# Kernel optimization log

Hardware: AMD Instinct MI355X
Metric: run time of the kernel (lower is better)

Reference implementation:

```python
import jax, jax.numpy as jnp
import numpy as np

V, EMB, H, N, E, B = 100000, 300, 64, 20000, 160000, 4096
L, T = 2, 3  # layer_timesteps = [3, 3]


def setup_inputs() -> dict:
    key = jax.random.key(0)
    ks = jax.random.split(key, 24)
    ri = lambda k, shape, hi: jax.random.randint(k, shape, 0, hi)
    rn = lambda k, shape, s=0.05: (jax.random.normal(k, shape, dtype=jnp.float32) * s)
    emb_table = rn(ks[7], (V, EMB), 0.1).at[0].set(0.0)  # padding_idx=0 row is zeros
    return {
        'emb_ind0': ri(ks[0], (N,), V),
        'emb_ind1': ri(ks[1], (N,), V),
        'adj0': ri(ks[2], (E, 2), N),
        'adj1': ri(ks[3], (E, 2), N),
        'prop_ind0': ri(ks[4], (B,), N),
        'prop_ind1': ri(ks[5], (B,), N),
        'labels': ri(ks[6], (B,), 2),
        'emb_table': emb_table,
        'proj_W': rn(ks[8], (EMB, H)),   # emb_proj weight (stored input-major)
        'proj_b': jnp.zeros((H,), jnp.float32),
        'msg_W': rn(ks[9], (L, H, H)),   # per-layer edge-type-0 message linear
        'msg_b': jnp.zeros((L, H), jnp.float32),
        'gru_Wih': rn(ks[10], (L, 3 * H, H)),
        'gru_Whh': rn(ks[11], (L, 3 * H, H)),
        'gru_bih': jnp.zeros((L, 3 * H), jnp.float32),
        'gru_bhh': jnp.zeros((L, 3 * H), jnp.float32),
        'cla_W1': rn(ks[12], (2 * H, 16)),
        'cla_b1': jnp.zeros((16,), jnp.float32),
        'cla_W2': rn(ks[13], (16, 1)),
        'cla_b2': jnp.zeros((1,), jnp.float32),
    }


def _gru_cell(x, h, Wih, Whh, bih, bhh):
    # torch.nn.GRUCell math
    gi = x @ Wih.T + bih
    gh = h @ Whh.T + bhh
    i_r, i_z, i_n = jnp.split(gi, 3, axis=-1)
    h_r, h_z, h_n = jnp.split(gh, 3, axis=-1)
    r = jax.nn.sigmoid(i_r + h_r)
    z = jax.nn.sigmoid(i_z + h_z)
    n = jnp.tanh(i_n + r * h_n)
    return (1.0 - z) * n + z * h


def reference(emb_ind0, emb_ind1, adj0, adj1, prop_ind0, prop_ind1, labels,
              emb_table, proj_W, proj_b, msg_W, msg_b,
              gru_Wih, gru_Whh, gru_bih, gru_bhh,
              cla_W1, cla_b1, cla_W2, cla_b2):
    def ggnn(x, adj):
        src, tgt = adj[:, 0], adj[:, 1]
        h = x
        for l in range(L):              # 2 structurally distinct layers
            for _ in range(T):          # 3 timesteps each
                m = h[src] @ msg_W[l] + msg_b[l]                     # [E, H] gather + transform
                inc = jax.ops.segment_sum(m, tgt, num_segments=N)    # scatter-add messages
                h = _gru_cell(inc, h, gru_Wih[l], gru_Whh[l], gru_bih[l], gru_bhh[l])
        return h

    def branch(emb_ind, adj, prop_ind):
        ge = emb_table[emb_ind]          # embedding lookup [N, EMB]
        ge = ge @ proj_W + proj_b        # emb_proj -> [N, H]
        ge = ggnn(ge, adj)
        return ge[prop_ind]              # index_select -> [B, H]

    g0 = branch(emb_ind0, adj0, prop_ind0)
    g1 = branch(emb_ind1, adj1, prop_ind1)
    ge = jnp.concatenate([g0, g1], axis=-1)                 # match='concat' -> [B, 2H]
    hid = jax.nn.relu(ge @ cla_W1 + cla_b1)
    logits = jax.nn.sigmoid(hid @ cla_W2 + cla_b2)          # [B, 1], num_class=1 path
    p = logits.squeeze(-1)
    y = labels.astype(p.dtype)
    eps = 1e-7  # mirrors torch BCELoss log-clamping
    loss = -jnp.mean(y * jnp.log(jnp.clip(p, eps, 1.0))
                     + (1.0 - y) * jnp.log(jnp.clip(1.0 - p, eps, 1.0)))
    return logits, loss
```

## Files before the change

### kernel.cpp

```cpp
#include <hip/hip_runtime.h>
#include <hip/hip_bf16.h>

typedef unsigned short u16;
typedef __attribute__((ext_vector_type(8))) short s16x8;
typedef __attribute__((ext_vector_type(4))) float f32x4;

#define NN 20000
#define HH 64
#define EMBD 300
#define EE 160000
#define BB 4096
#define NODES 40000

#define OFF_PROJB 0
#define OFF_MSGB  64
#define OFF_BIH   192
#define OFF_BHH   576
#define OFF_CW1T  960
#define OFF_CB1   3008
#define OFF_CW2   3024
#define OFF_CB2   3040
#define PARAM_SZ  3072

#define PB_WIH   0
#define PB_WHH   24576
#define PB_WMT   49152
#define PB_PROJT 57344
#define PB_SZ    77824

#define APAD 344

__device__ __forceinline__ float b2f(u16 u) {
    union { unsigned int i; float f; } v; v.i = ((unsigned int)u) << 16; return v.f;
}
__device__ __forceinline__ u16 f2b(float f) {
    union { float f; unsigned int u; } v; v.f = f;
    unsigned int u = v.u;
    return (u16)((u + 0x7FFFu + ((u >> 16) & 1u)) >> 16);
}
__device__ __forceinline__ float ldf(const void* p, long long i, int isbf) {
    return isbf ? b2f(((const u16*)p)[i]) : ((const float*)p)[i];
}
__device__ __forceinline__ u16 ldb(const void* p, long long i, int isbf) {
    return isbf ? ((const u16*)p)[i] : f2b(((const float*)p)[i]);
}
__device__ __forceinline__ void stf(void* p, long long i, int isbf, float v) {
    if (isbf) ((u16*)p)[i] = f2b(v);
    else      ((float*)p)[i] = v;
}

__global__ void sniff_kernel(const u16* probe, int* flag)
{
    if (threadIdx.x == 0 && blockIdx.x == 0) {
        int good = 0;
        for (int i = 0; i < 128; i += 2) {
            unsigned int e = (probe[i] >> 7) & 0xFF;
            if (e >= 105 && e <= 127) good++;
        }
        *flag = (good >= 48) ? 1 : 0;
    }
}

__global__ __launch_bounds__(256) void conv_kernel(
    const void* projW, const void* projb, const void* msgW, const void* msgb,
    const void* wih, const void* whh, const void* bih, const void* bhh,
    const void* cw1, const void* cb1, const void* cw2, const void* cb2,
    float* P, u16* PB, const int* flag)
{
    int isbf = *flag;
    int i = blockIdx.x * 256 + threadIdx.x;
    if (i < 64)    P[OFF_PROJB + i] = ldf(projb, i, isbf);
    if (i < 128)   P[OFF_MSGB + i]  = ldf(msgb, i, isbf);
    if (i < 384)   { P[OFF_BIH + i] = ldf(bih, i, isbf); P[OFF_BHH + i] = ldf(bhh, i, isbf); }
    if (i < 2048)  { int t = i >> 7, k = i & 127; P[OFF_CW1T + i] = ldf(cw1, (long long)k * 16 + t, isbf); }
    if (i < 16)    { P[OFF_CB1 + i] = ldf(cb1, i, isbf); P[OFF_CW2 + i] = ldf(cw2, i, isbf); }
    if (i == 0)    P[OFF_CB2] = ldf(cb2, 0, isbf);

    if (i < 24576) {
        int l = i / 12288, r = i - l * 12288;
        int frag = r >> 9, rr = r & 511, lane = rr >> 3, e = rr & 7;
        int jt = frag >> 1, kt = frag & 1;
        int srow = jt * 16 + (lane & 15);
        int sk = kt * 32 + ((lane >> 4) << 3) + e;
        long long si = (long long)l * 12288 + srow * 64 + sk;
        PB[PB_WIH + i] = ldb(wih, si, isbf);
        PB[PB_WHH + i] = ldb(whh, si, isbf);
    }
    if (i < 8192) {
        int l = i >> 12, r = i & 4095;
        int frag = r >> 9, rr = r & 511, lane = rr >> 3, e = rr & 7;
        int jt = frag >> 1, kt = frag & 1;
        int srow = jt * 16 + (lane & 15);
        int sk = kt * 32 + ((lane >> 4) << 3) + e;
        PB[PB_WMT + i] = ldb(msgW, (long long)l * 4096 + sk * 64 + srow, isbf);
    }
    if (i < 20480) {
        int frag = i >> 9, rr = i & 511, lane = rr >> 3, e = rr & 7;
        int jt = frag / 10, kt = frag - jt * 10;
        int srow = jt * 16 + (lane & 15);
        int sk = kt * 32 + ((lane >> 4) << 3) + e;
        PB[PB_PROJT + i] = (sk < 300) ? ldb(projW, (long long)sk * 64 + srow, isbf) : (u16)0;
    }
}

__global__ __launch_bounds__(256) void hist_kernel(const int* __restrict__ adj0,
                                                   const int* __restrict__ adj1, int* off)
{
    int e = blockIdx.x * 256 + threadIdx.x;
    if (e >= 2 * EE) return;
    int b = e / EE, le = e - b * EE;
    const int* adj = b ? adj1 : adj0;
    int tgt = adj[2 * le + 1];
    atomicAdd(&off[b * (NN + 1) + tgt + 1], 1);
}

__global__ __launch_bounds__(1024) void scan_kernel(int* off, int* cursor)
{
    int b = blockIdx.x;
    int* o = off + (size_t)b * (NN + 1);
    int* cur = cursor + (size_t)b * NN;
    __shared__ int wsum[16];
    __shared__ int wscan[16];
    int tid = threadIdx.x, wv = tid >> 6, lane = tid & 63;
    int base = 0;
    for (int start = 0; start < NN; start += 1024) {
        int i = start + tid;
        int v = (i < NN) ? o[i + 1] : 0;
        int orig = v;
        #pragma unroll
        for (int d = 1; d < 64; d <<= 1) {
            int t = __shfl_up(v, d);
            if (lane >= d) v += t;
        }
        if (lane == 63) wsum[wv] = v;
        __syncthreads();
        if (tid < 16) {
            int w = wsum[tid];
            #pragma unroll
            for (int d = 1; d < 16; d <<= 1) {
                int t = __shfl_up(w, d, 16);
                if (tid >= d) w += t;
            }
            wscan[tid] = w;
        }
        __syncthreads();
        int woff = (wv == 0) ? 0 : wscan[wv - 1];
        int excl = base + woff + v - orig;
        if (i < NN) { o[i] = excl; cur[i] = excl; }
        base += wscan[15];
    }
    if (tid == 0) o[NN] = base;
}

__global__ __launch_bounds__(256) void scatter_kernel(const int* __restrict__ adj0,
                                                      const int* __restrict__ adj1,
                                                      int* cursor, int* esrc)
{
    int e = blockIdx.x * 256 + threadIdx.x;
    if (e >= 2 * EE) return;
    int b = e / EE, le = e - b * EE;
    const int* adj = b ? adj1 : adj0;
    int src = adj[2 * le + 0];
    int tgt = adj[2 * le + 1];
    int pos = atomicAdd(&cursor[b * NN + tgt], 1);
    esrc[(size_t)b * EE + pos] = src;
}

__global__ __launch_bounds__(256) void projm_kernel(const void* emb,
                                                    const int* __restrict__ i0,
                                                    const int* __restrict__ i1,
                                                    const float* __restrict__ P,
                                                    const u16* __restrict__ PB,
                                                    u16* __restrict__ h, const int* flag)
{
    __shared__ u16 sA[64 * APAD];
    int isbf = *flag;
    int tid = threadIdx.x;
    int node0 = blockIdx.x * 64;

    {
        int r = tid >> 2, sub = tid & 3;
        int n = node0 + r;
        int b = n >= NN;
        int ln = n - b * NN;
        int idx = b ? i1[ln] : i0[ln];
        if (isbf) {
            const ushort4* src = (const ushort4*)((const u16*)emb + (size_t)idx * EMBD);
            ushort4* dst = (ushort4*)(sA + r * APAD);
            for (int c = sub; c < 75; c += 4) dst[c] = src[c];
            if (sub == 0) {
                ushort4 z = {0, 0, 0, 0};
                for (int c = 75; c < 80; ++c) dst[c] = z;
            }
        } else {
            const float* src = (const float*)emb + (size_t)idx * EMBD;
            for (int k = sub; k < 300; k += 4) sA[r * APAD + k] = f2b(src[k]);
            if (sub == 0) for (int k = 300; k < 320; ++k) sA[r * APAD + k] = 0;
        }
    }

    int wv = tid >> 6, lane = tid & 63, quad = lane >> 4, cn = lane & 15;
    int m0 = wv * 16;
    f32x4 acc[4];
    #pragma unroll
    for (int j = 0; j < 4; ++j) {
        float bb = P[OFF_PROJB + j * 16 + cn];
        acc[j] = {bb, bb, bb, bb};
    }
    #pragma unroll
    for (int kt = 0; kt < 10; ++kt) {
        s16x8 a = *(const s16x8*)&sA[(m0 + cn) * APAD + kt * 32 + quad * 8];
        #pragma unroll
        for (int j = 0; j < 4; ++j) {
            s16x8 bfr = *(const s16x8*)&PB[PB_PROJT + (j * 10 + kt) * 512 + lane * 8];
            acc[j] = __builtin_amdgcn_mfma_f32_16x16x32_bf16(a, bfr, acc[j], 0, 0, 0);
        }
    }
    #pragma unroll
    for (int j = 0; j < 4; ++j)
        #pragma unroll
        for (int r = 0; r < 4; ++r)
            h[(size_t)(node0 + m0 + quad * 4 + r) * 64 + j * 16 + cn] = f2b(acc[j][r]);
}

__global__ __launch_bounds__(256) void fstep_kernel(const u16* __restrict__ h_old,
                                                    u16* __restrict__ h_new,
                                                    const int* __restrict__ ioff,
                                                    const int* __restrict__ esrc,
                                                    const float* __restrict__ P,
                                                    const u16* __restrict__ PB, int l)
{
    __shared__ u16 s_S[32 * 64];
    __shared__ u16 s_h[32 * 64];
    __shared__ float s_deg[32];

    int tid = threadIdx.x;
    int node0 = blockIdx.x * 32;

    {
        int team = tid >> 3, oct = tid & 7;
        int node = node0 + team;
        int br = node >= NN;
        int ln = node - br * NN;
        const int* o = ioff + (size_t)br * (NN + 1);
        int s0 = o[ln], s1 = o[ln + 1];
        const int* es = esrc + (size_t)br * EE;
        const u16* hb = h_old + (size_t)br * NN * 64;

        float acc[8];
        #pragma unroll
        for (int k = 0; k < 8; ++k) acc[k] = 0.f;

        int base = s0, rem = s1 - s0;
        while (rem > 0) {
            int cnt = rem < 8 ? rem : 8;
            int myidx = es[base + (oct < cnt ? oct : cnt - 1)];
            #pragma unroll
            for (int j = 0; j < 8; ++j) {
                int e = __shfl(myidx, j, 8);
                uint4 v = *(const uint4*)&hb[(size_t)e * 64 + oct * 8];
                float w = (j < cnt) ? 1.f : 0.f;
                #pragma unroll
                for (int p = 0; p < 4; ++p) {
                    unsigned int u = ((const unsigned int*)&v)[p];
                    union { unsigned int i; float f; } lo, hi;
                    lo.i = u << 16; hi.i = u & 0xffff0000u;
                    acc[2 * p]     += w * lo.f;
                    acc[2 * p + 1] += w * hi.f;
                }
            }
            base += cnt;
            rem -= cnt;
        }

        u16 pk[8];
        #pragma unroll
        for (int k = 0; k < 8; ++k) pk[k] = f2b(acc[k]);
        *(uint4*)&s_S[team * 64 + oct * 8] = *(const uint4*)pk;
        *(uint4*)&s_h[team * 64 + oct * 8] =
            *(const uint4*)&h_old[(size_t)node * 64 + oct * 8];
        if (oct == 0) s_deg[team] = (float)(s1 - s0);
    }
    __syncthreads();

    int wv = tid >> 6, lane = tid & 63;
    int wr = wv >> 1, wc = wv & 1;
    int m0 = wr * 16;
    int quad = lane >> 4, cn = lane & 15;
    int arow = (m0 + cn) * 64 + quad * 8;
    int fl = lane * 8;

    s16x8 aS0 = *(const s16x8*)&s_S[arow];
    s16x8 aS1 = *(const s16x8*)&s_S[arow + 32];
    s16x8 aH0 = *(const s16x8*)&s_h[arow];
    s16x8 aH1 = *(const s16x8*)&s_h[arow + 32];
    __syncthreads();

    const u16* WM = PB + PB_WMT + (size_t)l * 4096;
    #pragma unroll
    for (int jtl = 0; jtl < 2; ++jtl) {
        int jt = wc * 2 + jtl;
        float mb = P[OFF_MSGB + l * 64 + jt * 16 + cn];
        f32x4 acc;
        acc[0] = s_deg[m0 + quad * 4 + 0] * mb;
        acc[1] = s_deg[m0 + quad * 4 + 1] * mb;
        acc[2] = s_deg[m0 + quad * 4 + 2] * mb;
        acc[3] = s_deg[m0 + quad * 4 + 3] * mb;
        acc = __builtin_amdgcn_mfma_f32_16x16x32_bf16(aS0, *(const s16x8*)&WM[(jt * 2 + 0) * 512 + fl], acc, 0, 0, 0);
        acc = __builtin_amdgcn_mfma_f32_16x16x32_bf16(aS1, *(const s16x8*)&WM[(jt * 2 + 1) * 512 + fl], acc, 0, 0, 0);
        #pragma unroll
        for (int r = 0; r < 4; ++r)
            s_S[(m0 + quad * 4 + r) * 64 + jt * 16 + cn] = f2b(acc[r]);
    }
    __syncthreads();

    s16x8 aI0 = *(const s16x8*)&s_S[arow];
    s16x8 aI1 = *(const s16x8*)&s_S[arow + 32];
    const u16* WI = PB + PB_WIH + (size_t)l * 12288;
    const u16* WH = PB + PB_WHH + (size_t)l * 12288;
    const float* bi = P + OFF_BIH + l * 192;
    const float* bh = P + OFF_BHH + l * 192;

    #pragma unroll
    for (int cl = 0; cl < 2; ++cl) {
        int jt = wc * 2 + cl;
        int j0 = jt * 16;
        float vr = bi[j0 + cn], vz = bi[64 + j0 + cn], vn = bi[128 + j0 + cn];
        float wr_ = bh[j0 + cn], wz = bh[64 + j0 + cn], wn = bh[128 + j0 + cn];
        f32x4 gr = {vr, vr, vr, vr}, gz = {vz, vz, vz, vz}, gn = {vn, vn, vn, vn};
        f32x4 hr = {wr_, wr_, wr_, wr_}, hz = {wz, wz, wz, wz}, hn = {wn, wn, wn, wn};
        int fr = (jt * 2) * 512 + fl, frz = ((4 + jt) * 2) * 512 + fl, frn = ((8 + jt) * 2) * 512 + fl;
        gr = __builtin_amdgcn_mfma_f32_16x16x32_bf16(aI0, *(const s16x8*)&WI[fr], gr, 0, 0, 0);
        gr = __builtin_amdgcn_mfma_f32_16x16x32_bf16(aI1, *(const s16x8*)&WI[fr + 512], gr, 0, 0, 0);
        gz = __builtin_amdgcn_mfma_f32_16x16x32_bf16(aI0, *(const s16x8*)&WI[frz], gz, 0, 0, 0);
        gz = __builtin_amdgcn_mfma_f32_16x16x32_bf16(aI1, *(const s16x8*)&WI[frz + 512], gz, 0, 0, 0);
        gn = __builtin_amdgcn_mfma_f32_16x16x32_bf16(aI0, *(const s16x8*)&WI[frn], gn, 0, 0, 0);
        gn = __builtin_amdgcn_mfma_f32_16x16x32_bf16(aI1, *(const s16x8*)&WI[frn + 512], gn, 0, 0, 0);
        hr = __builtin_amdgcn_mfma_f32_16x16x32_bf16(aH0, *(const s16x8*)&WH[fr], hr, 0, 0, 0);
        hr = __builtin_amdgcn_mfma_f32_16x16x32_bf16(aH1, *(const s16x8*)&WH[fr + 512], hr, 0, 0, 0);
        hz = __builtin_amdgcn_mfma_f32_16x16x32_bf16(aH0, *(const s16x8*)&WH[frz], hz, 0, 0, 0);
        hz = __builtin_amdgcn_mfma_f32_16x16x32_bf16(aH1, *(const s16x8*)&WH[frz + 512], hz, 0, 0, 0);
        hn = __builtin_amdgcn_mfma_f32_16x16x32_bf16(aH0, *(const s16x8*)&WH[frn], hn, 0, 0, 0);
        hn = __builtin_amdgcn_mfma_f32_16x16x32_bf16(aH1, *(const s16x8*)&WH[frn + 512], hn, 0, 0, 0);
        #pragma unroll
        for (int r = 0; r < 4; ++r) {
            int row = m0 + quad * 4 + r;
            float rr = 1.f / (1.f + __expf(-(gr[r] + hr[r])));
            float zz = 1.f / (1.f + __expf(-(gz[r] + hz[r])));
            float nn = tanhf(gn[r] + rr * hn[r]);
            float ho = b2f(s_h[row * 64 + j0 + cn]);
            h_new[(size_t)(node0 + row) * 64 + j0 + cn] = f2b((1.f - zz) * nn + zz * ho);
        }
    }
}

__global__ __launch_bounds__(256) void cls_kernel(const u16* __restrict__ h,
                                                  const int* __restrict__ p0,
                                                  const int* __restrict__ p1,
                                                  const int* __restrict__ labels,
                                                  const float* __restrict__ P,
                                                  void* out, float* partial, const int* flag)
{
    int isbf = *flag;
    int wv = threadIdx.x >> 6, lane = threadIdx.x & 63;
    int s = blockIdx.x * 4 + wv;
    int n0 = p0[s], n1 = p1[s];
    float f0 = b2f(h[(size_t)n0 * 64 + lane]);
    float f1 = b2f(h[(size_t)(NN + n1) * 64 + lane]);
    float z = P[OFF_CB2];
    #pragma unroll
    for (int t = 0; t < 16; ++t) {
        float part = f0 * P[OFF_CW1T + t * 128 + lane] + f1 * P[OFF_CW1T + t * 128 + 64 + lane];
        #pragma unroll
        for (int off = 32; off; off >>= 1) part += __shfl_xor(part, off);
        z += fmaxf(part + P[OFF_CB1 + t], 0.f) * P[OFF_CW2 + t];
    }
    float p = 1.f / (1.f + expf(-z));
    float y = (float)labels[s];
    const float eps = 1e-7f;
    float pc  = fminf(fmaxf(p, eps), 1.f);
    float pc1 = fminf(fmaxf(1.f - p, eps), 1.f);
    float term = y * logf(pc) + (1.f - y) * logf(pc1);
    __shared__ float red[4];
    if (lane == 0) { stf(out, s, isbf, p); red[wv] = term; }
    __syncthreads();
    if (threadIdx.x == 0) partial[blockIdx.x] = red[0] + red[1] + red[2] + red[3];
}

__global__ __launch_bounds__(256) void loss_kernel(const float* __restrict__ partial,
                                                   void* out, const int* flag)
{
    __shared__ float red[256];
    int tid = threadIdx.x;
    float s = 0.f;
    for (int i = tid; i < 1024; i += 256) s += partial[i];
    red[tid] = s;
    __syncthreads();
    for (int d = 128; d > 0; d >>= 1) {
        if (tid < d) red[tid] += red[tid + d];
        __syncthreads();
    }
    if (tid == 0) stf(out, BB, *flag, -red[0] / (float)BB);
}

extern "C" void kernel_launch(void* const* d_in, const int* in_sizes, int n_in,
                              void* d_out, int out_size, void* d_ws, size_t ws_size,
                              hipStream_t stream)
{
    const int* adj0   = (const int*)d_in[2];
    const int* adj1   = (const int*)d_in[3];
    const int* prop0  = (const int*)d_in[4];
    const int* prop1  = (const int*)d_in[5];
    const int* labels = (const int*)d_in[6];

    int* flag = (int*)d_ws;
    float* P  = (float*)d_ws + 16;
    u16* PB   = (u16*)(P + PARAM_SZ);
    u16* h0   = PB + PB_SZ;
    u16* h1   = h0 + (size_t)NODES * 64;
    float* partial = (float*)(h1 + (size_t)NODES * 64);
    int* ioff   = (int*)(partial + 1024);
    int* cursor = ioff + 2 * (NN + 1) + 62;
    int* esrc   = cursor + 2 * NN;

    hipMemsetAsync(ioff, 0, 2 * (NN + 1) * sizeof(int), stream);

    sniff_kernel<<<1, 64, 0, stream>>>((const u16*)d_in[8], flag);
    conv_kernel<<<96, 256, 0, stream>>>(d_in[8], d_in[9], d_in[10], d_in[11], d_in[12], d_in[13],
                                        d_in[14], d_in[15], d_in[16], d_in[17], d_in[18], d_in[19],
                                        P, PB, flag);
    hist_kernel<<<(2 * EE) / 256, 256, 0, stream>>>(adj0, adj1, ioff);
    scan_kernel<<<2, 1024, 0, stream>>>(ioff, cursor);
    scatter_kernel<<<(2 * EE) / 256, 256, 0, stream>>>(adj0, adj1, cursor, esrc);
    projm_kernel<<<(2 * NN) / 64, 256, 0, stream>>>(d_in[7], (const int*)d_in[0],
                                                    (const int*)d_in[1], P, PB, h0, flag);

    u16* hcur = h0;
    u16* hnext = h1;
    for (int l = 0; l < 2; ++l) {
        for (int t = 0; t < 3; ++t) {
            fstep_kernel<<<NODES / 32, 256, 0, stream>>>(hcur, hnext, ioff, esrc, P, PB, l);
            u16* tmp = hcur; hcur = hnext; hnext = tmp;
        }
    }

    cls_kernel<<<BB / 4, 256, 0, stream>>>(hcur, prop0, prop1, labels, P, d_out, partial, flag);
    loss_kernel<<<1, 256, 0, stream>>>(partial, d_out, flag);
}
```

Measured before the change: 397.7 us.

## Fuse six GGNN step launches into one cooperative persistent kernel with grid sync

Replaces the six per-timestep fstep launches with a single cooperative kernel of 625 blocks, each handling two 32-node tiles per step and separated by grid.sync. The goal is to remove kernel launch and drain overhead between timesteps. In exchange it lowers parallelism per step, since each block now processes its two tiles one after the other, and it adds a grid-wide barrier cost. It also depends on all 625 blocks being co-resident, which launch_bounds(256,3) is meant to allow. After six steps the final state sits in h0, so the classifier now reads h0.

```diff
diff --git a/kernel.cpp b/kernel.cpp
--- a/kernel.cpp
+++ b/kernel.cpp
@@ -1,5 +1,8 @@
 #include <hip/hip_runtime.h>
 #include <hip/hip_bf16.h>
+#include <hip/hip_cooperative_groups.h>
+
+namespace cg = cooperative_groups;
 
 typedef unsigned short u16;
 typedef __attribute__((ext_vector_type(8))) short s16x8;
@@ -223,66 +226,20 @@
             h[(size_t)(node0 + m0 + quad * 4 + r) * 64 + j * 16 + cn] = f2b(acc[j][r]);
 }
 
-__global__ __launch_bounds__(256) void fstep_kernel(const u16* __restrict__ h_old,
-                                                    u16* __restrict__ h_new,
-                                                    const int* __restrict__ ioff,
-                                                    const int* __restrict__ esrc,
-                                                    const float* __restrict__ P,
-                                                    const u16* __restrict__ PB, int l)
-{
+__global__ __launch_bounds__(256, 3) void floop_kernel(u16* __restrict__ h0,
+                                                       u16* __restrict__ h1,
+                                                       const int* __restrict__ ioff,
+                                                       const int* __restrict__ esrc,
+                                                       const float* __restrict__ P,
+                                                       const u16* __restrict__ PB)
+{
+    cg::grid_group grid = cg::this_grid();
+
     __shared__ u16 s_S[32 * 64];
     __shared__ u16 s_h[32 * 64];
     __shared__ float s_deg[32];
 
     int tid = threadIdx.x;
-    int node0 = blockIdx.x * 32;
-
-    {
-        int team = tid >> 3, oct = tid & 7;
-        int node = node0 + team;
-        int br = node >= NN;
-        int ln = node - br * NN;
-        const int* o = ioff + (size_t)br * (NN + 1);
-        int s0 = o[ln], s1 = o[ln + 1];
-        const int* es = esrc + (size_t)br * EE;
-        const u16* hb = h_old + (size_t)br * NN * 64;
-
-        float acc[8];
-        #pragma unroll
-        for (int k = 0; k < 8; ++k) acc[k] = 0.f;
-
-        int base = s0, rem = s1 - s0;
-        while (rem > 0) {
-            int cnt = rem < 8 ? rem : 8;
-            int myidx = es[base + (oct < cnt ? oct : cnt - 1)];
-            #pragma unroll
-            for (int j = 0; j < 8; ++j) {
-                int e = __shfl(myidx, j, 8);
-                uint4 v = *(const uint4*)&hb[(size_t)e * 64 + oct * 8];
-                float w = (j < cnt) ? 1.f : 0.f;
-                #pragma unroll
-                for (int p = 0; p < 4; ++p) {
-                    unsigned int u = ((const unsigned int*)&v)[p];
-                    union { unsigned int i; float f; } lo, hi;
-                    lo.i = u << 16; hi.i = u & 0xffff0000u;
-                    acc[2 * p]     += w * lo.f;
-                    acc[2 * p + 1] += w * hi.f;
-                }
-            }
-            base += cnt;
-            rem -= cnt;
-        }
-
-        u16 pk[8];
-        #pragma unroll
-        for (int k = 0; k < 8; ++k) pk[k] = f2b(acc[k]);
-        *(uint4*)&s_S[team * 64 + oct * 8] = *(const uint4*)pk;
-        *(uint4*)&s_h[team * 64 + oct * 8] =
-            *(const uint4*)&h_old[(size_t)node * 64 + oct * 8];
-        if (oct == 0) s_deg[team] = (float)(s1 - s0);
-    }
-    __syncthreads();
-
     int wv = tid >> 6, lane = tid & 63;
     int wr = wv >> 1, wc = wv & 1;
     int m0 = wr * 16;
@@ -290,67 +247,126 @@
     int arow = (m0 + cn) * 64 + quad * 8;
     int fl = lane * 8;
 
-    s16x8 aS0 = *(const s16x8*)&s_S[arow];
-    s16x8 aS1 = *(const s16x8*)&s_S[arow + 32];
-    s16x8 aH0 = *(const s16x8*)&s_h[arow];
-    s16x8 aH1 = *(const s16x8*)&s_h[arow + 32];
-    __syncthreads();
-
-    const u16* WM = PB + PB_WMT + (size_t)l * 4096;
-    #pragma unroll
-    for (int jtl = 0; jtl < 2; ++jtl) {
-        int jt = wc * 2 + jtl;
-        float mb = P[OFF_MSGB + l * 64 + jt * 16 + cn];
-        f32x4 acc;
-        acc[0] = s_deg[m0 + quad * 4 + 0] * mb;
-        acc[1] = s_deg[m0 + quad * 4 + 1] * mb;
-        acc[2] = s_deg[m0 + quad * 4 + 2] * mb;
-        acc[3] = s_deg[m0 + quad * 4 + 3] * mb;
-        acc = __builtin_amdgcn_mfma_f32_16x16x32_bf16(aS0, *(const s16x8*)&WM[(jt * 2 + 0) * 512 + fl], acc, 0, 0, 0);
-        acc = __builtin_amdgcn_mfma_f32_16x16x32_bf16(aS1, *(const s16x8*)&WM[(jt * 2 + 1) * 512 + fl], acc, 0, 0, 0);
-        #pragma unroll
-        for (int r = 0; r < 4; ++r)
-            s_S[(m0 + quad * 4 + r) * 64 + jt * 16 + cn] = f2b(acc[r]);
-    }
-    __syncthreads();
-
-    s16x8 aI0 = *(const s16x8*)&s_S[arow];
-    s16x8 aI1 = *(const s16x8*)&s_S[arow + 32];
-    const u16* WI = PB + PB_WIH + (size_t)l * 12288;
-    const u16* WH = PB + PB_WHH + (size_t)l * 12288;
-    const float* bi = P + OFF_BIH + l * 192;
-    const float* bh = P + OFF_BHH + l * 192;
-
-    #pragma unroll
-    for (int cl = 0; cl < 2; ++cl) {
-        int jt = wc * 2 + cl;
-        int j0 = jt * 16;
-        float vr = bi[j0 + cn], vz = bi[64 + j0 + cn], vn = bi[128 + j0 + cn];
-        float wr_ = bh[j0 + cn], wz = bh[64 + j0 + cn], wn = bh[128 + j0 + cn];
-        f32x4 gr = {vr, vr, vr, vr}, gz = {vz, vz, vz, vz}, gn = {vn, vn, vn, vn};
-        f32x4 hr = {wr_, wr_, wr_, wr_}, hz = {wz, wz, wz, wz}, hn = {wn, wn, wn, wn};
-        int fr = (jt * 2) * 512 + fl, frz = ((4 + jt) * 2) * 512 + fl, frn = ((8 + jt) * 2) * 512 + fl;
-        gr = __builtin_amdgcn_mfma_f32_16x16x32_bf16(aI0, *(const s16x8*)&WI[fr], gr, 0, 0, 0);
-        gr = __builtin_amdgcn_mfma_f32_16x16x32_bf16(aI1, *(const s16x8*)&WI[fr + 512], gr, 0, 0, 0);
-        gz = __builtin_amdgcn_mfma_f32_16x16x32_bf16(aI0, *(const s16x8*)&WI[frz], gz, 0, 0, 0);
-        gz = __builtin_amdgcn_mfma_f32_16x16x32_bf16(aI1, *(const s16x8*)&WI[frz + 512], gz, 0, 0, 0);
-        gn = __builtin_amdgcn_mfma_f32_16x16x32_bf16(aI0, *(const s16x8*)&WI[frn], gn, 0, 0, 0);
-        gn = __builtin_amdgcn_mfma_f32_16x16x32_bf16(aI1, *(const s16x8*)&WI[frn + 512], gn, 0, 0, 0);
-        hr = __builtin_amdgcn_mfma_f32_16x16x32_bf16(aH0, *(const s16x8*)&WH[fr], hr, 0, 0, 0);
-        hr = __builtin_amdgcn_mfma_f32_16x16x32_bf16(aH1, *(const s16x8*)&WH[fr + 512], hr, 0, 0, 0);
-        hz = __builtin_amdgcn_mfma_f32_16x16x32_bf16(aH0, *(const s16x8*)&WH[frz], hz, 0, 0, 0);
-        hz = __builtin_amdgcn_mfma_f32_16x16x32_bf16(aH1, *(const s16x8*)&WH[frz + 512], hz, 0, 0, 0);
-        hn = __builtin_amdgcn_mfma_f32_16x16x32_bf16(aH0, *(const s16x8*)&WH[frn], hn, 0, 0, 0);
-        hn = __builtin_amdgcn_mfma_f32_16x16x32_bf16(aH1, *(const s16x8*)&WH[frn + 512], hn, 0, 0, 0);
-        #pragma unroll
-        for (int r = 0; r < 4; ++r) {
-            int row = m0 + quad * 4 + r;
-            float rr = 1.f / (1.f + __expf(-(gr[r] + hr[r])));
-            float zz = 1.f / (1.f + __expf(-(gz[r] + hz[r])));
-            float nn = tanhf(gn[r] + rr * hn[r]);
-            float ho = b2f(s_h[row * 64 + j0 + cn]);
-            h_new[(size_t)(node0 + row) * 64 + j0 + cn] = f2b((1.f - zz) * nn + zz * ho);
-        }
+    for (int step = 0; step < 6; ++step) {
+        int l = (step >= 3) ? 1 : 0;
+        const u16* h_old = (step & 1) ? h1 : h0;
+        u16*       h_new = (step & 1) ? h0 : h1;
+
+        for (int tile = 0; tile < 2; ++tile) {
+            int node0 = (blockIdx.x * 2 + tile) * 32;
+
+            {
+                int team = tid >> 3, oct = tid & 7;
+                int node = node0 + team;
+                int br = node >= NN;
+                int ln = node - br * NN;
+                const int* o = ioff + (size_t)br * (NN + 1);
+                int s0 = o[ln], s1 = o[ln + 1];
+                const int* es = esrc + (size_t)br * EE;
+                const u16* hb = h_old + (size_t)br * NN * 64;
+
+                *(uint4*)&s_h[team * 64 + oct * 8] =
+                    *(const uint4*)&h_old[(size_t)node * 64 + oct * 8];
+                if (oct == 0) s_deg[team] = (float)(s1 - s0);
+
+                float acc[8];
+                #pragma unroll
+                for (int k = 0; k < 8; ++k) acc[k] = 0.f;
+
+                int base = s0, rem = s1 - s0;
+                while (rem > 0) {
+                    int cnt = rem < 8 ? rem : 8;
+                    int myidx = es[base + (oct < cnt ? oct : cnt - 1)];
+                    #pragma unroll
+                    for (int j = 0; j < 8; ++j) {
+                        int e = __shfl(myidx, j, 8);
+                        uint4 v = *(const uint4*)&hb[(size_t)e * 64 + oct * 8];
+                        float w = (j < cnt) ? 1.f : 0.f;
+                        #pragma unroll
+                        for (int p = 0; p < 4; ++p) {
+                            unsigned int u = ((const unsigned int*)&v)[p];
+                            union { unsigned int i; float f; } lo, hi;
+                            lo.i = u << 16; hi.i = u & 0xffff0000u;
+                            acc[2 * p]     += w * lo.f;
+                            acc[2 * p + 1] += w * hi.f;
+                        }
+                    }
+                    base += cnt;
+                    rem -= cnt;
+                }
+
+                u16 pk[8];
+                #pragma unroll
+                for (int k = 0; k < 8; ++k) pk[k] = f2b(acc[k]);
+                *(uint4*)&s_S[team * 64 + oct * 8] = *(const uint4*)pk;
+            }
+            __syncthreads();
+
+            s16x8 aS0 = *(const s16x8*)&s_S[arow];
+            s16x8 aS1 = *(const s16x8*)&s_S[arow + 32];
+            s16x8 aH0 = *(const s16x8*)&s_h[arow];
+            s16x8 aH1 = *(const s16x8*)&s_h[arow + 32];
+            __syncthreads();
+
+            const u16* WM = PB + PB_WMT + (size_t)l * 4096;
+            #pragma unroll
+            for (int jtl = 0; jtl < 2; ++jtl) {
+                int jt = wc * 2 + jtl;
+                float mb = P[OFF_MSGB + l * 64 + jt * 16 + cn];
+                f32x4 acc;
+                acc[0] = s_deg[m0 + quad * 4 + 0] * mb;
+                acc[1] = s_deg[m0 + quad * 4 + 1] * mb;
+                acc[2] = s_deg[m0 + quad * 4 + 2] * mb;
+                acc[3] = s_deg[m0 + quad * 4 + 3] * mb;
+                acc = __builtin_amdgcn_mfma_f32_16x16x32_bf16(aS0, *(const s16x8*)&WM[(jt * 2 + 0) * 512 + fl], acc, 0, 0, 0);
+                acc = __builtin_amdgcn_mfma_f32_16x16x32_bf16(aS1, *(const s16x8*)&WM[(jt * 2 + 1) * 512 + fl], acc, 0, 0, 0);
+                #pragma unroll
+                for (int r = 0; r < 4; ++r)
+                    s_S[(m0 + quad * 4 + r) * 64 + jt * 16 + cn] = f2b(acc[r]);
+            }
+            __syncthreads();
+
+            s16x8 aI0 = *(const s16x8*)&s_S[arow];
+            s16x8 aI1 = *(const s16x8*)&s_S[arow + 32];
+            const u16* WI = PB + PB_WIH + (size_t)l * 12288;
+            const u16* WH = PB + PB_WHH + (size_t)l * 12288;
+            const float* bi = P + OFF_BIH + l * 192;
+            const float* bh = P + OFF_BHH + l * 192;
+
+            #pragma unroll
+            for (int cl = 0; cl < 2; ++cl) {
+                int jt = wc * 2 + cl;
+                int j0 = jt * 16;
+                float vr = bi[j0 + cn], vz = bi[64 + j0 + cn], vn = bi[128 + j0 + cn];
+                float wr_ = bh[j0 + cn], wz = bh[64 + j0 + cn], wn = bh[128 + j0 + cn];
+                f32x4 gr = {vr, vr, vr, vr}, gz = {vz, vz, vz, vz}, gn = {vn, vn, vn, vn};
+                f32x4 hr = {wr_, wr_, wr_, wr_}, hz = {wz, wz, wz, wz}, hn = {wn, wn, wn, wn};
+                int fr = (jt * 2) * 512 + fl, frz = ((4 + jt) * 2) * 512 + fl, frn = ((8 + jt) * 2) * 512 + fl;
+                gr = __builtin_amdgcn_mfma_f32_16x16x32_bf16(aI0, *(const s16x8*)&WI[fr], gr, 0, 0, 0);
+                gr = __builtin_amdgcn_mfma_f32_16x16x32_bf16(aI1, *(const s16x8*)&WI[fr + 512], gr, 0, 0, 0);
+                gz = __builtin_amdgcn_mfma_f32_16x16x32_bf16(aI0, *(const s16x8*)&WI[frz], gz, 0, 0, 0);
+                gz = __builtin_amdgcn_mfma_f32_16x16x32_bf16(aI1, *(const s16x8*)&WI[frz + 512], gz, 0, 0, 0);
+                gn = __builtin_amdgcn_mfma_f32_16x16x32_bf16(aI0, *(const s16x8*)&WI[frn], gn, 0, 0, 0);
+                gn = __builtin_amdgcn_mfma_f32_16x16x32_bf16(aI1, *(const s16x8*)&WI[frn + 512], gn, 0, 0, 0);
+                hr = __builtin_amdgcn_mfma_f32_16x16x32_bf16(aH0, *(const s16x8*)&WH[fr], hr, 0, 0, 0);
+                hr = __builtin_amdgcn_mfma_f32_16x16x32_bf16(aH1, *(const s16x8*)&WH[fr + 512], hr, 0, 0, 0);
+                hz = __builtin_amdgcn_mfma_f32_16x16x32_bf16(aH0, *(const s16x8*)&WH[frz], hz, 0, 0, 0);
+                hz = __builtin_amdgcn_mfma_f32_16x16x32_bf16(aH1, *(const s16x8*)&WH[frz + 512], hz, 0, 0, 0);
+                hn = __builtin_amdgcn_mfma_f32_16x16x32_bf16(aH0, *(const s16x8*)&WH[frn], hn, 0, 0, 0);
+                hn = __builtin_amdgcn_mfma_f32_16x16x32_bf16(aH1, *(const s16x8*)&WH[frn + 512], hn, 0, 0, 0);
+                #pragma unroll
+                for (int r = 0; r < 4; ++r) {
+                    int row = m0 + quad * 4 + r;
+                    float rr = 1.f / (1.f + __expf(-(gr[r] + hr[r])));
+                    float zz = 1.f / (1.f + __expf(-(gz[r] + hz[r])));
+                    float nn = tanhf(gn[r] + rr * hn[r]);
+                    float ho = b2f(s_h[row * 64 + j0 + cn]);
+                    h_new[(size_t)(node0 + row) * 64 + j0 + cn] = f2b((1.f - zz) * nn + zz * ho);
+                }
+            }
+            __syncthreads();
+        }
+        grid.sync();
     }
 }
 
@@ -435,15 +451,13 @@
     projm_kernel<<<(2 * NN) / 64, 256, 0, stream>>>(d_in[7], (const int*)d_in[0],
                                                     (const int*)d_in[1], P, PB, h0, flag);
 
-    u16* hcur = h0;
-    u16* hnext = h1;
-    for (int l = 0; l < 2; ++l) {
-        for (int t = 0; t < 3; ++t) {
-            fstep_kernel<<<NODES / 32, 256, 0, stream>>>(hcur, hnext, ioff, esrc, P, PB, l);
-            u16* tmp = hcur; hcur = hnext; hnext = tmp;
-        }
-    }
-
-    cls_kernel<<<BB / 4, 256, 0, stream>>>(hcur, prop0, prop1, labels, P, d_out, partial, flag);
+    {
+        void* args[] = { (void*)&h0, (void*)&h1, (void*)&ioff, (void*)&esrc,
+                         (void*)&P, (void*)&PB };
+        hipLaunchCooperativeKernel((const void*)floop_kernel, dim3(625), dim3(256),
+                                   args, 0, stream);
+    }
+
+    cls_kernel<<<BB / 4, 256, 0, stream>>>(h0, prop0, prop1, labels, P, d_out, partial, flag);
     loss_kernel<<<1, 256, 0, stream>>>(partial, d_out, flag);
 }
```

Result: slower. 1.105 ms (+177.8%).
